# Optimization experiments

Measured on AMD Instinct MI355X. Metric: run time of the kernel, lower is better.

Reference implementation:

```python
import jax, jax.numpy as jnp
import numpy as np

HIDDEN = 1024

def setup_inputs() -> dict:
    key = jax.random.key(0)
    ks = jax.random.split(key, 7)
    scale = 1.0 / np.sqrt(HIDDEN)
    x = jax.random.normal(ks[0], (4, 2048, HIDDEN), dtype=jnp.float32)
    Wq = jax.random.uniform(ks[1], (HIDDEN, HIDDEN), jnp.float32, -scale, scale)
    bq = jax.random.uniform(ks[2], (HIDDEN,), jnp.float32, -scale, scale)
    Wk = jax.random.uniform(ks[3], (HIDDEN, HIDDEN), jnp.float32, -scale, scale)
    bk = jax.random.uniform(ks[4], (HIDDEN,), jnp.float32, -scale, scale)
    Wv = jax.random.uniform(ks[5], (HIDDEN, HIDDEN), jnp.float32, -scale, scale)
    bv = jax.random.uniform(ks[6], (HIDDEN,), jnp.float32, -scale, scale)
    return {"x": x, "Wq": Wq, "bq": bq, "Wk": Wk, "bk": bk, "Wv": Wv, "bv": bv}

def reference(x, Wq, bq, Wk, bk, Wv, bv):
    # x: [n, t, e]; weights stored as [in, out] so y = x @ W + b
    q = jnp.einsum('nte,ef->ntf', x, Wq) + bq
    k = jnp.einsum('nte,ef->ntf', x, Wk) + bk
    v = jnp.einsum('nte,ef->ntf', x, Wv) + bv
    scores = jnp.einsum('nqe,nke->nqk', q, k)  # unscaled, as in the original
    alpha = jax.nn.softmax(scores, axis=2)
    return jnp.einsum('nqk,nke->nqe', alpha, v)
```

## Files before the change

### kernel.cpp

```cpp
#include <hip/hip_runtime.h>
#include <stdint.h>

typedef __attribute__((ext_vector_type(4))) float f32x4;
typedef __attribute__((ext_vector_type(8))) _Float16 f16x8;
typedef __attribute__((ext_vector_type(8))) unsigned short u16x8;

#define HIDDEN 1024
#define SEQ 2048
#define NB 4

__device__ inline unsigned short f2h_bits(float f) {
    _Float16 h = (_Float16)f;
    return __builtin_bit_cast(unsigned short, h);
}
__device__ inline float h2f(unsigned short u) {
    return (float)__builtin_bit_cast(_Float16, u);
}

__device__ inline void gload16(const void* g, void* l) {
    __builtin_amdgcn_global_load_lds(
        (const __attribute__((address_space(1))) unsigned int*)g,
        (__attribute__((address_space(3))) unsigned int*)l,
        16, 0, 0);
}

template<int N> __device__ inline void waitvm() {
    if constexpr (N == 0) asm volatile("s_waitcnt vmcnt(0)" ::: "memory");
    else if constexpr (N == 3) asm volatile("s_waitcnt vmcnt(3)" ::: "memory");
    else if constexpr (N == 4) asm volatile("s_waitcnt vmcnt(4)" ::: "memory");
    else if constexpr (N == 6) asm volatile("s_waitcnt vmcnt(6)" ::: "memory");
    else if constexpr (N == 8) asm volatile("s_waitcnt vmcnt(8)" ::: "memory");
    else static_assert(N == 0, "bad vmcnt");
}
__device__ inline void waitlgkm0() { asm volatile("s_waitcnt lgkmcnt(0)" ::: "memory"); }

template<int BM, int BN, int WM, int WN, int BIAS_MODE, bool OUT_F16, int MINW>
__global__ __launch_bounds__(WM * WN * 64, MINW) void gemm8p(
    const unsigned short* __restrict__ A, int lda,
    const unsigned short* __restrict__ Bt, int ldb,
    const float* __restrict__ bias,
    void* __restrict__ Cptr, int ldc, int K,
    long long aBatch, long long bBatch, long long cBatch)
{
    constexpr int THREADS = WM * WN * 64;
    constexpr int MR = BM / (WM * 16);
    constexpr int NRW = BN / (WN * 16);
    constexpr int MH = MR / 2;
    constexpr int LA = 4 * BM / THREADS;
    constexpr int LB = 4 * BN / THREADS;
    constexpr int LP = LA + LB;
    constexpr int ASLICE = BM * 32;
    constexpr int BSLICE = BN * 32;
    constexpr int BOFF = 4 * ASLICE;

    extern __shared__ unsigned short lds[];

    const int tid = threadIdx.x, lane = tid & 63, wave = tid >> 6;
    const int wr = wave / WN, wc = wave % WN;
    const int fr = lane & 15, fq = lane >> 4;

    const int gx = gridDim.x, gy = gridDim.y;
    const int nwg = gx * gy * gridDim.z;
    const int id = (blockIdx.z * gy + blockIdx.y) * gx + blockIdx.x;
    const int id2 = (id & 7) * (nwg >> 3) + (id >> 3);
    const int bx = id2 % gx;
    const int by = (id2 / gx) % gy;
    const long long bz = id2 / (gx * gy);

    const unsigned short* Ab = A + bz * aBatch + (long long)(by * BM) * lda;
    const unsigned short* Bb = Bt + bz * bBatch + (long long)(bx * BN) * ldb;

    const unsigned short* sA[LA]; int dA[LA];
    #pragma unroll
    for (int i = 0; i < LA; ++i) {
        int c = i * THREADS + tid; int r = c >> 2; int ls = (c & 3) ^ ((r >> 1) & 3);
        sA[i] = Ab + (long long)r * lda + ls * 8;
        dA[i] = (i * THREADS + wave * 64) * 16;
    }
    const unsigned short* sB[LB]; int dB[LB];
    #pragma unroll
    for (int i = 0; i < LB; ++i) {
        int c = i * THREADS + tid; int r = c >> 2; int ls = (c & 3) ^ ((r >> 1) & 3);
        sB[i] = Bb + (long long)r * ldb + ls * 8;
        dB[i] = (i * THREADS + wave * 64) * 16;
    }

    auto stageA = [&](int q) {
        int slot = q & 3, kof = q * 32;
        #pragma unroll
        for (int i = 0; i < LA; ++i)
            gload16(sA[i] + kof, (char*)lds + slot * (ASLICE * 2) + dA[i]);
    };
    auto stageB = [&](int q) {
        int slot = q & 3, kof = q * 32;
        #pragma unroll
        for (int i = 0; i < LB; ++i)
            gload16(sB[i] + kof, (char*)lds + (BOFF + slot * BSLICE) * 2 + dB[i]);
    };

    const int NPAIR = K / 32;
    stageA(0); stageB(0); stageA(1); stageB(1); stageA(2); stageB(2);
    waitvm<2 * LP>();
    __builtin_amdgcn_s_barrier();

    f32x4 acc[MR][NRW] = {};

    for (int p = 0; p < NPAIR; ++p) {
        const int slot = p & 3;
        const unsigned short* as = lds + slot * ASLICE;
        const unsigned short* bs = lds + BOFF + slot * BSLICE;
        f16x8 af[MR], bf[NRW];

        #pragma unroll
        for (int n = 0; n < NRW; ++n) {
            int r = wc * (BN / WN) + n * 16 + fr;
            int es = fq ^ ((r >> 1) & 3);
            bf[n] = *(const f16x8*)&bs[r * 32 + es * 8];
        }
        #pragma unroll
        for (int m = 0; m < MH; ++m) {
            int r = wr * (BM / WM) + m * 16 + fr;
            int es = fq ^ ((r >> 1) & 3);
            af[m] = *(const f16x8*)&as[r * 32 + es * 8];
        }
        if (p + 3 < NPAIR) stageA(p + 3);
        __builtin_amdgcn_s_barrier();
        waitlgkm0();
        __builtin_amdgcn_sched_barrier(0);
        __builtin_amdgcn_s_setprio(1);
        #pragma unroll
        for (int m = 0; m < MH; ++m)
            #pragma unroll
            for (int n = 0; n < NRW; ++n)
                acc[m][n] = __builtin_amdgcn_mfma_f32_16x16x32_f16(af[m], bf[n], acc[m][n], 0, 0, 0);
        __builtin_amdgcn_s_setprio(0);
        __builtin_amdgcn_s_barrier();

        #pragma unroll
        for (int m = MH; m < MR; ++m) {
            int r = wr * (BM / WM) + m * 16 + fr;
            int es = fq ^ ((r >> 1) & 3);
            af[m] = *(const f16x8*)&as[r * 32 + es * 8];
        }
        if (p + 3 < NPAIR) stageB(p + 3);
        __builtin_amdgcn_s_barrier();
        waitlgkm0();
        __builtin_amdgcn_sched_barrier(0);
        __builtin_amdgcn_s_setprio(1);
        #pragma unroll
        for (int m = MH; m < MR; ++m)
            #pragma unroll
            for (int n = 0; n < NRW; ++n)
                acc[m][n] = __builtin_amdgcn_mfma_f32_16x16x32_f16(af[m], bf[n], acc[m][n], 0, 0, 0);
        __builtin_amdgcn_s_setprio(0);
        if (p < NPAIR - 3) waitvm<2 * LP>();
        else if (p == NPAIR - 3) waitvm<LP>();
        else if (p == NPAIR - 2) waitvm<0>();
        __builtin_amdgcn_s_barrier();
    }

    const int row0 = by * BM + wr * (BM / WM);
    const int col0 = bx * BN + wc * (BN / WN);
    #pragma unroll
    for (int m = 0; m < MR; ++m)
        #pragma unroll
        for (int n = 0; n < NRW; ++n)
            #pragma unroll
            for (int i = 0; i < 4; ++i) {
                int r = row0 + m * 16 + fq * 4 + i;
                int c = col0 + n * 16 + fr;
                float v = acc[m][n][i];
                if constexpr (BIAS_MODE == 1) v += bias[c];
                if constexpr (BIAS_MODE == 2) v += bias[r];
                if constexpr (OUT_F16)
                    ((unsigned short*)Cptr + bz * cBatch)[(long long)r * ldc + c] = f2h_bits(v);
                else
                    ((float*)Cptr + bz * cBatch)[(long long)r * ldc + c] = v;
            }
}

__global__ __launch_bounds__(256) void cvt_f32_f16(const float* __restrict__ in,
                                                   unsigned short* __restrict__ out, int n8)
{
    int i = blockIdx.x * blockDim.x + threadIdx.x;
    if (i >= n8) return;
    const float4* p = (const float4*)in + (long long)i * 2;
    float4 a = p[0], b = p[1];
    ushort4 o0, o1;
    o0.x = f2h_bits(a.x); o0.y = f2h_bits(a.y); o0.z = f2h_bits(a.z); o0.w = f2h_bits(a.w);
    o1.x = f2h_bits(b.x); o1.y = f2h_bits(b.y); o1.z = f2h_bits(b.z); o1.w = f2h_bits(b.w);
    ushort4* o = (ushort4*)out + (long long)i * 2;
    o[0] = o0; o[1] = o1;
}

__global__ void transpose_cvt(const float* __restrict__ in, unsigned short* __restrict__ out,
                              int R, int C)
{
    __shared__ unsigned short t[32][33];
    const int bx = blockIdx.x * 32;
    const int by = blockIdx.y * 32;
    const int xT = threadIdx.x, yT = threadIdx.y;
    #pragma unroll
    for (int i = 0; i < 32; i += 8)
        t[yT + i][xT] = f2h_bits(in[(long long)(by + yT + i) * C + bx + xT]);
    __syncthreads();
    #pragma unroll
    for (int i = 0; i < 32; i += 8)
        out[(long long)(bx + yT + i) * R + by + xT] = t[xT][yT + i];
}

__global__ void concat_bias2(const float* __restrict__ bq, const float* __restrict__ bk,
                             float* __restrict__ cb)
{
    int i = threadIdx.x;
    cb[i] = bq[i];
    cb[HIDDEN + i] = bk[i];
}

__global__ __launch_bounds__(256) void softmax_h(unsigned short* __restrict__ S)
{
    const int tid = threadIdx.x;
    unsigned short* row = S + (long long)blockIdx.x * SEQ;
    u16x8 hv = *(const u16x8*)&row[tid * 8];
    float vv[8];
    #pragma unroll
    for (int j = 0; j < 8; ++j) vv[j] = h2f(hv[j]);

    float mx = vv[0];
    #pragma unroll
    for (int j = 1; j < 8; ++j) mx = fmaxf(mx, vv[j]);
    #pragma unroll
    for (int o = 32; o > 0; o >>= 1) mx = fmaxf(mx, __shfl_xor(mx, o));
    __shared__ float redm[4], reds[4];
    if ((tid & 63) == 0) redm[tid >> 6] = mx;
    __syncthreads();
    mx = fmaxf(fmaxf(redm[0], redm[1]), fmaxf(redm[2], redm[3]));

    float ev[8], sum = 0.f;
    #pragma unroll
    for (int j = 0; j < 8; ++j) { ev[j] = __expf(vv[j] - mx); sum += ev[j]; }
    #pragma unroll
    for (int o = 32; o > 0; o >>= 1) sum += __shfl_xor(sum, o);
    if ((tid & 63) == 0) reds[tid >> 6] = sum;
    __syncthreads();
    sum = reds[0] + reds[1] + reds[2] + reds[3];
    float inv = 1.0f / sum;

    u16x8 ov;
    #pragma unroll
    for (int j = 0; j < 8; ++j) ov[j] = f2h_bits(ev[j] * inv);
    *(u16x8*)&row[tid * 8] = ov;
}

extern "C" void kernel_launch(void* const* d_in, const int* in_sizes, int n_in,
                              void* d_out, int out_size, void* d_ws, size_t ws_size,
                              hipStream_t stream)
{
    (void)in_sizes; (void)n_in; (void)out_size; (void)ws_size;
    const float* x  = (const float*)d_in[0];
    const float* Wq = (const float*)d_in[1];
    const float* bq = (const float*)d_in[2];
    const float* Wk = (const float*)d_in[3];
    const float* bk = (const float*)d_in[4];
    const float* Wv = (const float*)d_in[5];
    const float* bv = (const float*)d_in[6];
    float* out = (float*)d_out;

    (void)hipFuncSetAttribute(reinterpret_cast<const void*>(&gemm8p<256, 256, 2, 4, 1, true, 2>),
                              hipFuncAttributeMaxDynamicSharedMemorySize, 131072);
    (void)hipFuncSetAttribute(reinterpret_cast<const void*>(&gemm8p<256, 256, 2, 4, 0, true, 2>),
                              hipFuncAttributeMaxDynamicSharedMemorySize, 131072);
    (void)hipFuncSetAttribute(reinterpret_cast<const void*>(&gemm8p<128, 256, 2, 4, 2, true, 2>),
                              hipFuncAttributeMaxDynamicSharedMemorySize, 98304);
    (void)hipFuncSetAttribute(reinterpret_cast<const void*>(&gemm8p<256, 128, 2, 4, 0, false, 2>),
                              hipFuncAttributeMaxDynamicSharedMemorySize, 98304);

    char* ws = (char*)d_ws;
    const long long MTOT = (long long)NB * SEQ;

    unsigned short* qk = (unsigned short*)ws;
    unsigned short* vt = (unsigned short*)(ws + (size_t)MTOT * 2048 * 2);
    char* sreg = ws + (size_t)MTOT * 2048 * 2 + (size_t)HIDDEN * MTOT * 2;
    unsigned short* wt = (unsigned short*)sreg;
    float* cb = (float*)(sreg + (size_t)3 * HIDDEN * HIDDEN * 2);
    unsigned short* xh = (unsigned short*)(sreg + (size_t)3 * HIDDEN * HIDDEN * 2 + 8192);
    unsigned short* S = (unsigned short*)sreg;

    {
        int n8 = (int)(MTOT * HIDDEN / 8);
        cvt_f32_f16<<<dim3((n8 + 255) / 256), 256, 0, stream>>>(x, xh, n8);
    }
    dim3 tb(32, 8), tg(HIDDEN / 32, HIDDEN / 32);
    transpose_cvt<<<tg, tb, 0, stream>>>(Wq, wt,                       HIDDEN, HIDDEN);
    transpose_cvt<<<tg, tb, 0, stream>>>(Wk, wt +     HIDDEN * HIDDEN, HIDDEN, HIDDEN);
    transpose_cvt<<<tg, tb, 0, stream>>>(Wv, wt + 2 * HIDDEN * HIDDEN, HIDDEN, HIDDEN);
    concat_bias2<<<1, 1024, 0, stream>>>(bq, bk, cb);

    gemm8p<256, 256, 2, 4, 1, true, 2><<<dim3(2048 / 256, (unsigned)(MTOT / 256), 1), 512, 131072, stream>>>(
        xh, HIDDEN, wt, HIDDEN, cb, qk, 2048, HIDDEN, 0, 0, 0);

    gemm8p<128, 256, 2, 4, 2, true, 2><<<dim3((unsigned)(MTOT / 256), HIDDEN / 128, 1), 512, 98304, stream>>>(
        wt + 2 * HIDDEN * HIDDEN, HIDDEN, xh, HIDDEN, bv, vt, (int)MTOT, HIDDEN, 0, 0, 0);

    gemm8p<256, 256, 2, 4, 0, true, 2><<<dim3(SEQ / 256, SEQ / 256, NB), 512, 131072, stream>>>(
        qk, 2048, qk + HIDDEN, 2048, nullptr, S, SEQ, HIDDEN,
        (long long)SEQ * 2048, (long long)SEQ * 2048, (long long)SEQ * SEQ);

    softmax_h<<<dim3(NB * SEQ), 256, 0, stream>>>(S);

    gemm8p<256, 128, 2, 4, 0, false, 2><<<dim3(HIDDEN / 128, SEQ / 256, NB), 512, 98304, stream>>>(
        S, SEQ, vt, (int)MTOT, nullptr, out, HIDDEN, SEQ,
        (long long)SEQ * SEQ, (long long)SEQ, (long long)SEQ * HIDDEN);
}
```

Baseline: 181.3 us.

## Register double-buffer LDS fragments and unify GEMMs on 256x128 tiles

Replaces the split-half A/B staging loop with a single-stage-per-k-slice pipeline. Fragments for the next slice are read from LDS into a second register set while MFMAs run on the current one, and global loads are issued four slices ahead. All four GEMMs now use one fixed 256x128 tile with 96KB LDS instead of mixing 256x256 and 128x256 tiles. This removes one barrier per slice and hides LDS latency, at the cost of more registers and smaller tiles for the QK and projection GEMMs.

```diff
diff --git a/kernel.cpp b/kernel.cpp
--- a/kernel.cpp
+++ b/kernel.cpp
@@ -27,25 +27,23 @@
 template<int N> __device__ inline void waitvm() {
     if constexpr (N == 0) asm volatile("s_waitcnt vmcnt(0)" ::: "memory");
     else if constexpr (N == 3) asm volatile("s_waitcnt vmcnt(3)" ::: "memory");
-    else if constexpr (N == 4) asm volatile("s_waitcnt vmcnt(4)" ::: "memory");
     else if constexpr (N == 6) asm volatile("s_waitcnt vmcnt(6)" ::: "memory");
-    else if constexpr (N == 8) asm volatile("s_waitcnt vmcnt(8)" ::: "memory");
     else static_assert(N == 0, "bad vmcnt");
 }
 __device__ inline void waitlgkm0() { asm volatile("s_waitcnt lgkmcnt(0)" ::: "memory"); }
 
-template<int BM, int BN, int WM, int WN, int BIAS_MODE, bool OUT_F16, int MINW>
-__global__ __launch_bounds__(WM * WN * 64, MINW) void gemm8p(
+template<int BIAS_MODE, bool OUT_F16>
+__global__ __launch_bounds__(512, 2) void gemmrr(
     const unsigned short* __restrict__ A, int lda,
     const unsigned short* __restrict__ Bt, int ldb,
     const float* __restrict__ bias,
     void* __restrict__ Cptr, int ldc, int K,
     long long aBatch, long long bBatch, long long cBatch)
 {
-    constexpr int THREADS = WM * WN * 64;
+    constexpr int BM = 256, BN = 128, WM = 2, WN = 4;
+    constexpr int THREADS = 512;
     constexpr int MR = BM / (WM * 16);
     constexpr int NRW = BN / (WN * 16);
-    constexpr int MH = MR / 2;
     constexpr int LA = 4 * BM / THREADS;
     constexpr int LB = 4 * BN / THREADS;
     constexpr int LP = LA + LB;
@@ -85,78 +83,68 @@
         dB[i] = (i * THREADS + wave * 64) * 16;
     }
 
-    auto stageA = [&](int q) {
+    auto stage = [&](int q) {
         int slot = q & 3, kof = q * 32;
         #pragma unroll
         for (int i = 0; i < LA; ++i)
             gload16(sA[i] + kof, (char*)lds + slot * (ASLICE * 2) + dA[i]);
-    };
-    auto stageB = [&](int q) {
-        int slot = q & 3, kof = q * 32;
         #pragma unroll
         for (int i = 0; i < LB; ++i)
             gload16(sB[i] + kof, (char*)lds + (BOFF + slot * BSLICE) * 2 + dB[i]);
     };
 
-    const int NPAIR = K / 32;
-    stageA(0); stageB(0); stageA(1); stageB(1); stageA(2); stageB(2);
-    waitvm<2 * LP>();
-    __builtin_amdgcn_s_barrier();
-
-    f32x4 acc[MR][NRW] = {};
-
-    for (int p = 0; p < NPAIR; ++p) {
-        const int slot = p & 3;
+    auto rdfrags = [&](int q, f16x8 (&af)[MR], f16x8 (&bf)[NRW]) {
+        int slot = q & 3;
         const unsigned short* as = lds + slot * ASLICE;
         const unsigned short* bs = lds + BOFF + slot * BSLICE;
-        f16x8 af[MR], bf[NRW];
-
+        #pragma unroll
+        for (int m = 0; m < MR; ++m) {
+            int r = wr * (BM / WM) + m * 16 + fr;
+            int es = fq ^ ((r >> 1) & 3);
+            af[m] = *(const f16x8*)&as[r * 32 + es * 8];
+        }
         #pragma unroll
         for (int n = 0; n < NRW; ++n) {
             int r = wc * (BN / WN) + n * 16 + fr;
             int es = fq ^ ((r >> 1) & 3);
             bf[n] = *(const f16x8*)&bs[r * 32 + es * 8];
         }
-        #pragma unroll
-        for (int m = 0; m < MH; ++m) {
-            int r = wr * (BM / WM) + m * 16 + fr;
-            int es = fq ^ ((r >> 1) & 3);
-            af[m] = *(const f16x8*)&as[r * 32 + es * 8];
-        }
-        if (p + 3 < NPAIR) stageA(p + 3);
-        __builtin_amdgcn_s_barrier();
+    };
+
+    const int NPAIR = K / 32;
+    stage(0); stage(1); stage(2); stage(3);
+    waitvm<2 * LP>();
+    __builtin_amdgcn_s_barrier();
+
+    f32x4 acc[MR][NRW] = {};
+    f16x8 afA[MR], bfA[NRW], afB[MR], bfB[NRW];
+    rdfrags(0, afA, bfA);
+    waitlgkm0();
+    __builtin_amdgcn_sched_barrier(0);
+
+    auto slice = [&](int p, f16x8 (&afc)[MR], f16x8 (&bfc)[NRW],
+                     f16x8 (&afn)[MR], f16x8 (&bfn)[NRW]) {
+        if (p + 1 < NPAIR) rdfrags(p + 1, afn, bfn);
+        if (p + 4 < NPAIR) stage(p + 4);
+        __builtin_amdgcn_sched_barrier(0);
+        __builtin_amdgcn_s_setprio(1);
+        #pragma unroll
+        for (int m = 0; m < MR; ++m)
+            #pragma unroll
+            for (int n = 0; n < NRW; ++n)
+                acc[m][n] = __builtin_amdgcn_mfma_f32_16x16x32_f16(afc[m], bfc[n], acc[m][n], 0, 0, 0);
+        __builtin_amdgcn_s_setprio(0);
         waitlgkm0();
         __builtin_amdgcn_sched_barrier(0);
-        __builtin_amdgcn_s_setprio(1);
-        #pragma unroll
-        for (int m = 0; m < MH; ++m)
-            #pragma unroll
-            for (int n = 0; n < NRW; ++n)
-                acc[m][n] = __builtin_amdgcn_mfma_f32_16x16x32_f16(af[m], bf[n], acc[m][n], 0, 0, 0);
-        __builtin_amdgcn_s_setprio(0);
+        if (p <= NPAIR - 5) waitvm<2 * LP>();
+        else if (p == NPAIR - 4) waitvm<LP>();
+        else waitvm<0>();
         __builtin_amdgcn_s_barrier();
-
-        #pragma unroll
-        for (int m = MH; m < MR; ++m) {
-            int r = wr * (BM / WM) + m * 16 + fr;
-            int es = fq ^ ((r >> 1) & 3);
-            af[m] = *(const f16x8*)&as[r * 32 + es * 8];
-        }
-        if (p + 3 < NPAIR) stageB(p + 3);
-        __builtin_amdgcn_s_barrier();
-        waitlgkm0();
-        __builtin_amdgcn_sched_barrier(0);
-        __builtin_amdgcn_s_setprio(1);
-        #pragma unroll
-        for (int m = MH; m < MR; ++m)
-            #pragma unroll
-            for (int n = 0; n < NRW; ++n)
-                acc[m][n] = __builtin_amdgcn_mfma_f32_16x16x32_f16(af[m], bf[n], acc[m][n], 0, 0, 0);
-        __builtin_amdgcn_s_setprio(0);
-        if (p < NPAIR - 3) waitvm<2 * LP>();
-        else if (p == NPAIR - 3) waitvm<LP>();
-        else if (p == NPAIR - 2) waitvm<0>();
-        __builtin_amdgcn_s_barrier();
+    };
+
+    for (int p = 0; p < NPAIR; p += 2) {
+        slice(p,     afA, bfA, afB, bfB);
+        slice(p + 1, afB, bfB, afA, bfA);
     }
 
     const int row0 = by * BM + wr * (BM / WM);
@@ -266,13 +254,13 @@
     const float* bv = (const float*)d_in[6];
     float* out = (float*)d_out;
 
-    (void)hipFuncSetAttribute(reinterpret_cast<const void*>(&gemm8p<256, 256, 2, 4, 1, true, 2>),
-                              hipFuncAttributeMaxDynamicSharedMemorySize, 131072);
-    (void)hipFuncSetAttribute(reinterpret_cast<const void*>(&gemm8p<256, 256, 2, 4, 0, true, 2>),
-                              hipFuncAttributeMaxDynamicSharedMemorySize, 131072);
-    (void)hipFuncSetAttribute(reinterpret_cast<const void*>(&gemm8p<128, 256, 2, 4, 2, true, 2>),
+    (void)hipFuncSetAttribute(reinterpret_cast<const void*>(&gemmrr<1, true>),
                               hipFuncAttributeMaxDynamicSharedMemorySize, 98304);
-    (void)hipFuncSetAttribute(reinterpret_cast<const void*>(&gemm8p<256, 128, 2, 4, 0, false, 2>),
+    (void)hipFuncSetAttribute(reinterpret_cast<const void*>(&gemmrr<2, true>),
+                              hipFuncAttributeMaxDynamicSharedMemorySize, 98304);
+    (void)hipFuncSetAttribute(reinterpret_cast<const void*>(&gemmrr<0, true>),
+                              hipFuncAttributeMaxDynamicSharedMemorySize, 98304);
+    (void)hipFuncSetAttribute(reinterpret_cast<const void*>(&gemmrr<0, false>),
                               hipFuncAttributeMaxDynamicSharedMemorySize, 98304);
 
     char* ws = (char*)d_ws;
@@ -296,19 +284,19 @@
     transpose_cvt<<<tg, tb, 0, stream>>>(Wv, wt + 2 * HIDDEN * HIDDEN, HIDDEN, HIDDEN);
     concat_bias2<<<1, 1024, 0, stream>>>(bq, bk, cb);
 
-    gemm8p<256, 256, 2, 4, 1, true, 2><<<dim3(2048 / 256, (unsigned)(MTOT / 256), 1), 512, 131072, stream>>>(
+    gemmrr<1, true><<<dim3(2048 / 128, (unsigned)(MTOT / 256), 1), 512, 98304, stream>>>(
         xh, HIDDEN, wt, HIDDEN, cb, qk, 2048, HIDDEN, 0, 0, 0);
 
-    gemm8p<128, 256, 2, 4, 2, true, 2><<<dim3((unsigned)(MTOT / 256), HIDDEN / 128, 1), 512, 98304, stream>>>(
+    gemmrr<2, true><<<dim3((unsigned)(MTOT / 128), HIDDEN / 256, 1), 512, 98304, stream>>>(
         wt + 2 * HIDDEN * HIDDEN, HIDDEN, xh, HIDDEN, bv, vt, (int)MTOT, HIDDEN, 0, 0, 0);
 
-    gemm8p<256, 256, 2, 4, 0, true, 2><<<dim3(SEQ / 256, SEQ / 256, NB), 512, 131072, stream>>>(
+    gemmrr<0, true><<<dim3(SEQ / 128, SEQ / 256, NB), 512, 98304, stream>>>(
         qk, 2048, qk + HIDDEN, 2048, nullptr, S, SEQ, HIDDEN,
         (long long)SEQ * 2048, (long long)SEQ * 2048, (long long)SEQ * SEQ);
 
     softmax_h<<<dim3(NB * SEQ), 256, 0, stream>>>(S);
 
-    gemm8p<256, 128, 2, 4, 0, false, 2><<<dim3(HIDDEN / 128, SEQ / 256, NB), 512, 98304, stream>>>(
+    gemmrr<0, false><<<dim3(HIDDEN / 128, SEQ / 256, NB), 512, 98304, stream>>>(
         S, SEQ, vt, (int)MTOT, nullptr, out, HIDDEN, SEQ,
         (long long)SEQ * SEQ, (long long)SEQ, (long long)SEQ * HIDDEN);
 }
```

Result: slower. 198.2 us (+9.3%).
